# Kernel optimization log

Hardware: AMD Instinct MI355X
Metric: run time of the kernel (lower is better)

## Reference

```python
import jax, jax.numpy as jnp
import numpy as np

N = 50000      # nodes
E = 800000     # edges (avg degree 16)
F_IN = 128
HID = 128
C = 40
EPS = 1e-5     # BatchNorm1d eps


def setup_inputs() -> dict:
    key = jax.random.key(0)
    ks = jax.random.split(key, 8)

    def glorot(k, shape):
        lim = np.sqrt(6.0 / (shape[0] + shape[1])).astype(np.float32)
        return jax.random.uniform(k, shape, jnp.float32, -lim, lim)

    inp = {
        "features": jax.random.normal(ks[0], (N, F_IN), jnp.float32),
        "edge_index": jax.random.randint(ks[1], (2, E), 0, N, jnp.int32),
        "W1": glorot(ks[2], (F_IN, HID)), "b1": jnp.zeros((HID,), jnp.float32),
        "gamma1": jnp.ones((HID,), jnp.float32), "beta1": jnp.zeros((HID,), jnp.float32),
        "W2": glorot(ks[3], (HID, HID)), "b2": jnp.zeros((HID,), jnp.float32),
        "gamma2": jnp.ones((HID,), jnp.float32), "beta2": jnp.zeros((HID,), jnp.float32),
        "W3": glorot(ks[4], (HID, C)), "b3": jnp.zeros((C,), jnp.float32),
    }
    return inp


def _gcn_norm(edge_index):
    # Add self-loops and compute symmetric normalization D^-1/2 (A+I) D^-1/2
    loops = jnp.arange(N, dtype=edge_index.dtype)
    src = jnp.concatenate([edge_index[0], loops])
    dst = jnp.concatenate([edge_index[1], loops])
    deg = jax.ops.segment_sum(jnp.ones((E + N,), jnp.float32), dst, num_segments=N)
    dinv = jax.lax.rsqrt(jnp.maximum(deg, 1.0))
    return src, dst, dinv[src] * dinv[dst]  # per-edge norm coefficient


def _gcn_conv(x, W, b, src, dst, norm):
    h = x @ W                                   # [N, out]
    msg = h[src] * norm[:, None]                # gather + scale, [E+N, out]
    return jax.ops.segment_sum(msg, dst, num_segments=N) + b


def _bn(x, gamma, beta):
    # training-mode BatchNorm1d over the node axis (biased variance)
    mu = jnp.mean(x, axis=0)
    var = jnp.mean(jnp.square(x - mu), axis=0)
    return (x - mu) * jax.lax.rsqrt(var + EPS) * gamma + beta


def reference(features, edge_index, W1, b1, gamma1, beta1, W2, b2, gamma2, beta2, W3, b3):
    src, dst, norm = _gcn_norm(edge_index)
    h = jax.nn.relu(_bn(_gcn_conv(features, W1, b1, src, dst, norm), gamma1, beta1))
    h = jax.nn.relu(_bn(_gcn_conv(h, W2, b2, src, dst, norm), gamma2, beta2))
    h = _gcn_conv(h, W3, b3, src, dst, norm)
    return jax.nn.log_softmax(h, axis=-1)
```

## Files before the change

kernel.cpp:

```cpp
#include <hip/hip_runtime.h>
#include <math.h>

#define FEAT 128
#define NCLS 40
#define BN_EPS 1e-5f
#define CAP 64

typedef unsigned short u16;
typedef unsigned int u32;
typedef __attribute__((ext_vector_type(8))) short bf16x8;
typedef __attribute__((ext_vector_type(4))) float f32x4;

__device__ inline u32 f2b2(float a, float b) {
    u32 ua = __float_as_uint(a), ub = __float_as_uint(b);
    ua = (ua + 0x7fffu + ((ua >> 16) & 1u)) >> 16;
    ub = (ub + 0x7fffu + ((ub >> 16) & 1u)) >> 16;
    return ua | (ub << 16);
}
__device__ inline u16 f2b1(float a) {
    u32 ua = __float_as_uint(a);
    return (u16)((ua + 0x7fffu + ((ua >> 16) & 1u)) >> 16);
}
__device__ inline float b2f(u16 u) { return __uint_as_float((u32)u << 16); }
__device__ inline float4 b4fv(ushort4 u) {
    return make_float4(b2f(u.x), b2f(u.y), b2f(u.z), b2f(u.w));
}
__device__ inline float blo(u32 u) { return __uint_as_float(u << 16); }
__device__ inline float bhi(u32 u) { return __uint_as_float(u & 0xffff0000u); }

__device__ inline void b8acc(uint4 u, float w, float* a) {
    a[0] = fmaf(w, blo(u.x), a[0]); a[1] = fmaf(w, bhi(u.x), a[1]);
    a[2] = fmaf(w, blo(u.y), a[2]); a[3] = fmaf(w, bhi(u.y), a[3]);
    a[4] = fmaf(w, blo(u.z), a[4]); a[5] = fmaf(w, bhi(u.z), a[5]);
    a[6] = fmaf(w, blo(u.w), a[6]); a[7] = fmaf(w, bhi(u.w), a[7]);
}


__device__ inline void stage_wt(const float* __restrict__ W, u16* Wt) {
    const float4* W4 = (const float4*)W;
#pragma unroll
    for (int i = 0; i < 16; ++i) {
        int li = threadIdx.x + i * 256;
        int k = li >> 5;
        int n0 = (li & 31) * 4;
        int s = k >> 5, quad = (k >> 3) & 3, koff = k & 7;
        int nt = n0 >> 4, nl0 = n0 & 15;
        int base = ((s * 8 + nt) * 64 + quad * 16) * 8 + koff;
        float4 w = W4[li];
        Wt[base + (nl0 + 0) * 8] = f2b1(w.x);
        Wt[base + (nl0 + 1) * 8] = f2b1(w.y);
        Wt[base + (nl0 + 2) * 8] = f2b1(w.z);
        Wt[base + (nl0 + 3) * 8] = f2b1(w.w);
    }
}

__global__ __launch_bounds__(256) void k_pack(const float* __restrict__ W1,
                                              const float* __restrict__ W2,
                                              u16* __restrict__ Wg) {
    const float* W = (blockIdx.x == 0) ? W1 : W2;
    stage_wt(W, Wg + (size_t)blockIdx.x * 128 * 128);
}

__device__ inline void mfma_core(const u16* __restrict__ Wt, const bf16x8* bfrag,
                                 u16* __restrict__ Y, int node, int M, int nl, int quad) {
    int lane = quad * 16 + nl;
    f32x4 acc[8];
#pragma unroll
    for (int nt = 0; nt < 8; ++nt) acc[nt] = (f32x4){0.f, 0.f, 0.f, 0.f};
#pragma unroll
    for (int s = 0; s < 4; ++s) {
#pragma unroll
        for (int nt = 0; nt < 8; ++nt) {
            uint4 aw = ((const uint4*)Wt)[(s * 8 + nt) * 64 + lane];
            bf16x8 af = *(bf16x8*)&aw;
            acc[nt] = __builtin_amdgcn_mfma_f32_16x16x32_bf16(af, bfrag[s], acc[nt], 0, 0, 0);
        }
    }
    if (node < M) {
#pragma unroll
        for (int nt = 0; nt < 8; ++nt) {
            uint2 o;
            o.x = f2b2(acc[nt][0], acc[nt][1]);
            o.y = f2b2(acc[nt][2], acc[nt][3]);
            *(uint2*)&Y[(size_t)node * 128 + nt * 16 + quad * 4] = o;
        }
    }
}


__global__ __launch_bounds__(256, 8) void k_l1_fill(
    const float* __restrict__ X, const u16* __restrict__ Wg, u16* __restrict__ Y, int M,
    const int* __restrict__ src, const int* __restrict__ dst,
    int* __restrict__ cnt, u16* __restrict__ col, int E,
    int gemmBlocks, int nchunks)
{
    if ((int)blockIdx.x < gemmBlocks) {
        int wv = threadIdx.x >> 6;
        int lane = threadIdx.x & 63;
        int nl = lane & 15, quad = lane >> 4;
        int node = blockIdx.x * 64 + wv * 16 + nl;

        bf16x8 bfrag[4];
        if (node < M) {
            const float4* xr = (const float4*)(X + (size_t)node * 128);
#pragma unroll
            for (int s = 0; s < 4; ++s) {
                float4 xa = xr[s * 8 + quad * 2];
                float4 xb = xr[s * 8 + quad * 2 + 1];
                uint4 bu;
                bu.x = f2b2(xa.x, xa.y); bu.y = f2b2(xa.z, xa.w);
                bu.z = f2b2(xb.x, xb.y); bu.w = f2b2(xb.z, xb.w);
                bfrag[s] = *(bf16x8*)&bu;
            }
        } else {
            uint4 z = make_uint4(0, 0, 0, 0);
#pragma unroll
            for (int s = 0; s < 4; ++s) bfrag[s] = *(bf16x8*)&z;
        }
        mfma_core(Wg, bfrag, Y, node, M, nl, quad);
    } else {
        int fb = blockIdx.x - gemmBlocks;
        int part = fb & 7;
        int chunk = fb >> 3;
        int lo = (int)(((long long)M * part) >> 3);
        int hi = (int)(((long long)M * (part + 1)) >> 3);
        int per = ((E + nchunks - 1) / nchunks + 7) & ~7;
        int e0 = chunk * per;
        int e1 = e0 + per; if (e1 > E) e1 = E;

        for (int eb = e0 + (int)threadIdx.x * 8; eb < e1; eb += 2048) {
            if (eb + 8 <= e1) {
                int4 da = *(const int4*)(dst + eb);
                int4 db = *(const int4*)(dst + eb + 4);
                int4 sa = *(const int4*)(src + eb);
                int4 sb = *(const int4*)(src + eb + 4);
                int dd[8] = {da.x, da.y, da.z, da.w, db.x, db.y, db.z, db.w};
                int ss[8] = {sa.x, sa.y, sa.z, sa.w, sb.x, sb.y, sb.z, sb.w};
#pragma unroll
                for (int k = 0; k < 8; ++k) {
                    int d = dd[k];
                    if (d >= lo && d < hi) {
                        int c = atomicAdd(&cnt[d], 1);
                        if (c < CAP) col[(size_t)d * CAP + c] = (u16)ss[k];
                    }
                }
            } else {
                for (int e = eb; e < e1; ++e) {
                    int d = dst[e];
                    if (d >= lo && d < hi) {
                        int c = atomicAdd(&cnt[d], 1);
                        if (c < CAP) col[(size_t)d * CAP + c] = (u16)src[e];
                    }
                }
            }
        }
    }
}


__global__ __launch_bounds__(256) void k_mfma_l2(
    const u16* __restrict__ X, const u16* __restrict__ Wg,
    const float* __restrict__ sums, const float* __restrict__ gamma,
    const float* __restrict__ beta, u16* __restrict__ Y, int M)
{
    __shared__ __align__(16) float scs[128], shs[128];

    if (threadIdx.x < 128) {
        int f = threadIdx.x;
        float inv_n = 1.f / (float)M;
        float mu = sums[f] * inv_n;
        float var = sums[128 + f] * inv_n - mu * mu;
        float rs = rsqrtf(var + BN_EPS);
        float sc = gamma[f] * rs;
        scs[f] = sc;
        shs[f] = beta[f] - mu * sc;
    }
    __syncthreads();

    int wv = threadIdx.x >> 6;
    int lane = threadIdx.x & 63;
    int nl = lane & 15, quad = lane >> 4;
    int node = blockIdx.x * 64 + wv * 16 + nl;

    bf16x8 bfrag[4];
    if (node < M) {
        const uint4* xr = (const uint4*)(X + (size_t)node * 128);
#pragma unroll
        for (int s = 0; s < 4; ++s) {
            int k0 = s * 32 + quad * 8;
            uint4 xu = xr[s * 4 + quad];
            float4 sc0 = *(const float4*)&scs[k0];
            float4 sc1 = *(const float4*)&scs[k0 + 4];
            float4 sh0 = *(const float4*)&shs[k0];
            float4 sh1 = *(const float4*)&shs[k0 + 4];
            float v0 = fmaxf(fmaf(blo(xu.x), sc0.x, sh0.x), 0.f);
            float v1 = fmaxf(fmaf(bhi(xu.x), sc0.y, sh0.y), 0.f);
            float v2 = fmaxf(fmaf(blo(xu.y), sc0.z, sh0.z), 0.f);
            float v3 = fmaxf(fmaf(bhi(xu.y), sc0.w, sh0.w), 0.f);
            float v4 = fmaxf(fmaf(blo(xu.z), sc1.x, sh1.x), 0.f);
            float v5 = fmaxf(fmaf(bhi(xu.z), sc1.y, sh1.y), 0.f);
            float v6 = fmaxf(fmaf(blo(xu.w), sc1.z, sh1.z), 0.f);
            float v7 = fmaxf(fmaf(bhi(xu.w), sc1.w, sh1.w), 0.f);
            uint4 bu;
            bu.x = f2b2(v0, v1); bu.y = f2b2(v2, v3);
            bu.z = f2b2(v4, v5); bu.w = f2b2(v6, v7);
            bfrag[s] = *(bf16x8*)&bu;
        }
    } else {
        uint4 z = make_uint4(0, 0, 0, 0);
#pragma unroll
        for (int s = 0; s < 4; ++s) bfrag[s] = *(bf16x8*)&z;
    }
    mfma_core(Wg, bfrag, Y, node, M, nl, quad);
}


__global__ __launch_bounds__(256) void k_gemm40(
    const u16* __restrict__ X, const float* __restrict__ W,
    const float* __restrict__ sums, const float* __restrict__ gamma,
    const float* __restrict__ beta, u16* __restrict__ Y, int M)
{
    __shared__ float Ws[128 * 40];
    __shared__ __align__(16) float scs[128], shs[128];
    __shared__ float Xs[32 * 260];

    int t = threadIdx.x;
    int row0 = blockIdx.x * 256;
    int tx = t & 3, ty = t >> 2;

    if (t < 128) {
        float inv_n = 1.f / (float)M;
        float mu = sums[t] * inv_n;
        float var = sums[128 + t] * inv_n - mu * mu;
        float rs = rsqrtf(var + BN_EPS);
        float sc = gamma[t] * rs;
        scs[t] = sc;
        shs[t] = beta[t] - mu * sc;
    }
    {
        const float4* W4 = (const float4*)W;
        float4* Ws4 = (float4*)Ws;
#pragma unroll
        for (int i = 0; i < 5; ++i) Ws4[t + i * 256] = W4[t + i * 256];
    }

    float acc[4][10];
#pragma unroll
    for (int r = 0; r < 4; ++r)
#pragma unroll
        for (int c = 0; c < 10; ++c) acc[r][c] = 0.f;

    for (int k0 = 0; k0 < 128; k0 += 32) {
        __syncthreads();
        {
            int rr = t >> 3;
            int kc = (t & 7) * 4;
            float4 sc = *(const float4*)&scs[k0 + kc];
            float4 sh = *(const float4*)&shs[k0 + kc];
#pragma unroll
            for (int p = 0; p < 8; ++p) {
                int r = rr + p * 32;
                int grow = row0 + r;
                float4 v = make_float4(0.f, 0.f, 0.f, 0.f);
                if (grow < M) v = b4fv(*(const ushort4*)(X + (size_t)grow * 128 + k0 + kc));
                v.x = fmaxf(fmaf(v.x, sc.x, sh.x), 0.f);
                v.y = fmaxf(fmaf(v.y, sc.y, sh.y), 0.f);
                v.z = fmaxf(fmaf(v.z, sc.z, sh.z), 0.f);
                v.w = fmaxf(fmaf(v.w, sc.w, sh.w), 0.f);
                Xs[(kc + 0) * 260 + r] = v.x;
                Xs[(kc + 1) * 260 + r] = v.y;
                Xs[(kc + 2) * 260 + r] = v.z;
                Xs[(kc + 3) * 260 + r] = v.w;
            }
        }
        __syncthreads();
#pragma unroll 8
        for (int kk = 0; kk < 32; ++kk) {
            const float4 xv = *(const float4*)&Xs[kk * 260 + ty * 4];
            const float xr[4] = {xv.x, xv.y, xv.z, xv.w};
            float wc[10];
#pragma unroll
            for (int c = 0; c < 5; ++c) {
                float2 w2 = *(const float2*)&Ws[(k0 + kk) * 40 + tx * 10 + c * 2];
                wc[c * 2] = w2.x; wc[c * 2 + 1] = w2.y;
            }
#pragma unroll
            for (int r = 0; r < 4; ++r)
#pragma unroll
                for (int c = 0; c < 10; ++c)
                    acc[r][c] = fmaf(xr[r], wc[c], acc[r][c]);
        }
    }

#pragma unroll
    for (int r = 0; r < 4; ++r) {
        int grow = row0 + ty * 4 + r;
        if (grow < M) {
            u32* yp = (u32*)(Y + (size_t)grow * 40 + tx * 10);
#pragma unroll
            for (int c = 0; c < 5; ++c)
                yp[c] = f2b2(acc[r][c * 2], acc[r][c * 2 + 1]);
        }
    }
}


__global__ __launch_bounds__(256) void k_agg128(
    const u16* __restrict__ t, const int* __restrict__ cnt,
    const u16* __restrict__ col, const float* __restrict__ bias,
    u16* __restrict__ out, int n)
{
    int wid = threadIdx.x >> 4;
    int lane = threadIdx.x & 15;
    int i = blockIdx.x * 16 + wid;
    if (i >= n) return;
    int c = cnt[i];
    int deg = c < CAP ? c : CAP;
    int beg = i * CAP, end = beg + deg;
    float di = rsqrtf((float)(c + 1));

    float a[8];
    {
        uint4 su = ((const uint4*)(t + (size_t)i * 128))[lane];
        a[0] = di * blo(su.x); a[1] = di * bhi(su.x);
        a[2] = di * blo(su.y); a[3] = di * bhi(su.y);
        a[4] = di * blo(su.z); a[5] = di * bhi(su.z);
        a[6] = di * blo(su.w); a[7] = di * bhi(su.w);
    }

    int j = beg;
    for (; j + 7 < end; j += 8) {
        int s[8]; int sc[8]; uint4 v[8];
#pragma unroll
        for (int k = 0; k < 8; ++k) s[k] = (int)col[j + k];
#pragma unroll
        for (int k = 0; k < 8; ++k) {
            sc[k] = cnt[s[k]];
            v[k] = ((const uint4*)(t + (size_t)s[k] * 128))[lane];
        }
#pragma unroll
        for (int k = 0; k < 8; ++k) b8acc(v[k], rsqrtf((float)(sc[k] + 1)), a);
    }
    for (; j < end; ++j) {
        int s0 = (int)col[j];
        float w0 = rsqrtf((float)(cnt[s0] + 1));
        uint4 v = ((const uint4*)(t + (size_t)s0 * 128))[lane];
        b8acc(v, w0, a);
    }

    float4 bA = ((const float4*)bias)[lane * 2];
    float4 bB = ((const float4*)bias)[lane * 2 + 1];
    uint4 o;
    o.x = f2b2(fmaf(di, a[0], bA.x), fmaf(di, a[1], bA.y));
    o.y = f2b2(fmaf(di, a[2], bA.z), fmaf(di, a[3], bA.w));
    o.z = f2b2(fmaf(di, a[4], bB.x), fmaf(di, a[5], bB.y));
    o.w = f2b2(fmaf(di, a[6], bB.z), fmaf(di, a[7], bB.w));
    ((uint4*)(out + (size_t)i * 128))[lane] = o;
}


__global__ __launch_bounds__(256) void k_bnstats(const u16* __restrict__ a,
                                                 float* __restrict__ sums, int n) {
    int lane = threadIdx.x & 15;
    int rt = threadIdx.x >> 4;
    float s[8], q[8];
#pragma unroll
    for (int k = 0; k < 8; ++k) { s[k] = 0.f; q[k] = 0.f; }

    for (int i = blockIdx.x * 16 + rt; i < n; i += gridDim.x * 16) {
        uint4 u = ((const uint4*)(a + (size_t)i * 128))[lane];
        float v[8] = {blo(u.x), bhi(u.x), blo(u.y), bhi(u.y),
                      blo(u.z), bhi(u.z), blo(u.w), bhi(u.w)};
#pragma unroll
        for (int k = 0; k < 8; ++k) { s[k] += v[k]; q[k] = fmaf(v[k], v[k], q[k]); }
    }

    __shared__ float red[16][128];
#pragma unroll
    for (int k = 0; k < 8; ++k) red[rt][lane * 8 + k] = s[k];
    __syncthreads();
    if (threadIdx.x < 128) {
        float v = 0.f;
#pragma unroll
        for (int w = 0; w < 16; ++w) v += red[w][threadIdx.x];
        atomicAdd(&sums[threadIdx.x], v);
    }
    __syncthreads();
#pragma unroll
    for (int k = 0; k < 8; ++k) red[rt][lane * 8 + k] = q[k];
    __syncthreads();
    if (threadIdx.x < 128) {
        float v = 0.f;
#pragma unroll
        for (int w = 0; w < 16; ++w) v += red[w][threadIdx.x];
        atomicAdd(&sums[128 + threadIdx.x], v);
    }
}


__global__ __launch_bounds__(256) void k_agg40(
    const u16* __restrict__ t, const int* __restrict__ cnt,
    const u16* __restrict__ col, const float* __restrict__ bias,
    float* __restrict__ out, int n)
{
    int i = blockIdx.x * 32 + (threadIdx.x >> 3);
    if (i >= n) return;
    int l = threadIdx.x & 7;
    bool act = l < 5;
    int c = cnt[i];
    int deg = c < CAP ? c : CAP;
    int beg = i * CAP, end = beg + deg;
    float di = rsqrtf((float)(c + 1));

    float a[8] = {0.f, 0.f, 0.f, 0.f, 0.f, 0.f, 0.f, 0.f};
    if (act) {
        uint4 su = ((const uint4*)(t + (size_t)i * NCLS))[l];
        a[0] = di * blo(su.x); a[1] = di * bhi(su.x);
        a[2] = di * blo(su.y); a[3] = di * bhi(su.y);
        a[4] = di * blo(su.z); a[5] = di * bhi(su.z);
        a[6] = di * blo(su.w); a[7] = di * bhi(su.w);
    }
    int j = beg;
    for (; j + 7 < end; j += 8) {
        int s[8]; int sc[8]; uint4 v[8];
#pragma unroll
        for (int k = 0; k < 8; ++k) s[k] = (int)col[j + k];
#pragma unroll
        for (int k = 0; k < 8; ++k) {
            sc[k] = cnt[s[k]];
            v[k] = act ? ((const uint4*)(t + (size_t)s[k] * NCLS))[l]
                       : make_uint4(0, 0, 0, 0);
        }
#pragma unroll
        for (int k = 0; k < 8; ++k) b8acc(v[k], rsqrtf((float)(sc[k] + 1)), a);
    }
    for (; j < end; ++j) {
        int s0 = (int)col[j];
        float w0 = rsqrtf((float)(cnt[s0] + 1));
        uint4 v = act ? ((const uint4*)(t + (size_t)s0 * NCLS))[l]
                      : make_uint4(0, 0, 0, 0);
        b8acc(v, w0, a);
    }

    float v[8];
    float m = -INFINITY;
    if (act) {
        float4 b0 = *(const float4*)(bias + l * 8);
        float4 b1 = *(const float4*)(bias + l * 8 + 4);
        v[0] = fmaf(di, a[0], b0.x); v[1] = fmaf(di, a[1], b0.y);
        v[2] = fmaf(di, a[2], b0.z); v[3] = fmaf(di, a[3], b0.w);
        v[4] = fmaf(di, a[4], b1.x); v[5] = fmaf(di, a[5], b1.y);
        v[6] = fmaf(di, a[6], b1.z); v[7] = fmaf(di, a[7], b1.w);
#pragma unroll
        for (int k = 0; k < 8; ++k) m = fmaxf(m, v[k]);
    }
#pragma unroll
    for (int d = 1; d < 8; d <<= 1) m = fmaxf(m, __shfl_xor(m, d, 8));
    float es = 0.f;
    if (act) {
#pragma unroll
        for (int k = 0; k < 8; ++k) es += expf(v[k] - m);
    }
#pragma unroll
    for (int d = 1; d < 8; d <<= 1) es += __shfl_xor(es, d, 8);
    float ls = logf(es);
    if (act) {
        float4 o0, o1;
        o0.x = v[0] - m - ls; o0.y = v[1] - m - ls;
        o0.z = v[2] - m - ls; o0.w = v[3] - m - ls;
        o1.x = v[4] - m - ls; o1.y = v[5] - m - ls;
        o1.z = v[6] - m - ls; o1.w = v[7] - m - ls;
        *(float4*)(out + (size_t)i * NCLS + l * 8) = o0;
        *(float4*)(out + (size_t)i * NCLS + l * 8 + 4) = o1;
    }
}


extern "C" void kernel_launch(void* const* d_in, const int* in_sizes, int n_in,
                              void* d_out, int out_size, void* d_ws, size_t ws_size,
                              hipStream_t stream) {
    const float* features = (const float*)d_in[0];
    const int* edge_index = (const int*)d_in[1];
    const float* W1 = (const float*)d_in[2];
    const float* b1 = (const float*)d_in[3];
    const float* gamma1 = (const float*)d_in[4];
    const float* beta1 = (const float*)d_in[5];
    const float* W2 = (const float*)d_in[6];
    const float* b2 = (const float*)d_in[7];
    const float* gamma2 = (const float*)d_in[8];
    const float* beta2 = (const float*)d_in[9];
    const float* W3 = (const float*)d_in[10];
    const float* b3 = (const float*)d_in[11];
    float* out = (float*)d_out;

    int n = in_sizes[0] / FEAT;
    int E = in_sizes[1] / 2;

    char* p = (char*)d_ws;
    auto alloc = [&](size_t bytes) -> void* {
        void* r = (void*)p;
        p += (bytes + 255) & ~(size_t)255;
        return r;
    };
    int* cnt     = (int*)alloc((size_t)n * 4);
    float* sums  = (float*)alloc(512 * 4);
    size_t zspan = (size_t)((char*)(sums + 512) - (char*)cnt);
    u16* colb    = (u16*)alloc((size_t)n * CAP * 2);
    u16* hb      = (u16*)alloc((size_t)n * 128 * 2);
    u16* ab      = (u16*)alloc((size_t)n * 128 * 2);
    u16* wgb     = (u16*)alloc((size_t)2 * 128 * 128 * 2);

    float* sums1 = sums;
    float* sums2 = sums + 256;
    u16* Wg1 = wgb;
    u16* Wg2 = wgb + 128 * 128;

    const int* e_src = edge_index;
    const int* e_dst = edge_index + E;

    int gb64 = (n + 63) / 64;
    int gb16 = (n + 15) / 16;
    int gb32 = (n + 31) / 32;

    hipMemsetAsync(cnt, 0, zspan, stream);
    k_pack<<<2, 256, 0, stream>>>(W1, W2, wgb);

    int nchunks = 160;
    k_l1_fill<<<gb64 + nchunks * 8, 256, 0, stream>>>(features, Wg1, hb, n,
                                                      e_src, e_dst, cnt, colb, E,
                                                      gb64, nchunks);

    k_agg128<<<gb16, 256, 0, stream>>>(hb, cnt, colb, b1, ab, n);
    k_bnstats<<<512, 256, 0, stream>>>(ab, sums1, n);

    k_mfma_l2<<<gb64, 256, 0, stream>>>(ab, Wg2, sums1, gamma1, beta1, hb, n);
    k_agg128<<<gb16, 256, 0, stream>>>(hb, cnt, colb, b2, ab, n);
    k_bnstats<<<512, 256, 0, stream>>>(ab, sums2, n);

    k_gemm40<<<(n + 255) / 256, 256, 0, stream>>>(ab, W3, sums2, gamma2, beta2, hb, n);
    k_agg40<<<gb32, 256, 0, stream>>>(hb, cnt, colb, b3, out, n);
}
```

Baseline: 332.0 us.

## Fuse BN stats into aggregation, MFMA layer-3 GEMM, merge init kernels

BatchNorm sum and sum-of-squares accumulation moves into the 128-wide aggregation kernel, which becomes grid-stride over a capped grid. This drops the separate stats pass that re-read the activations. The fp32 scalar layer-3 GEMM is replaced by a bf16 MFMA kernel using a pre-packed, zero-padded W3. The memset and weight packing are merged into one init kernel, and layer-2 weights are staged in LDS. The capped grid reduces parallelism in the aggregation and adds more atomic contention per block, and bf16 on layer 3 changes numerics slightly.

```diff
diff --git a/kernel.cpp b/kernel.cpp
--- a/kernel.cpp
+++ b/kernel.cpp
@@ -22,9 +22,6 @@
     return (u16)((ua + 0x7fffu + ((ua >> 16) & 1u)) >> 16);
 }
 __device__ inline float b2f(u16 u) { return __uint_as_float((u32)u << 16); }
-__device__ inline float4 b4fv(ushort4 u) {
-    return make_float4(b2f(u.x), b2f(u.y), b2f(u.z), b2f(u.w));
-}
 __device__ inline float blo(u32 u) { return __uint_as_float(u << 16); }
 __device__ inline float bhi(u32 u) { return __uint_as_float(u & 0xffff0000u); }
 
@@ -54,14 +51,35 @@
     }
 }
 
-__global__ __launch_bounds__(256) void k_pack(const float* __restrict__ W1,
-                                              const float* __restrict__ W2,
-                                              u16* __restrict__ Wg) {
-    const float* W = (blockIdx.x == 0) ? W1 : W2;
-    stage_wt(W, Wg + (size_t)blockIdx.x * 128 * 128);
-}
-
-__device__ inline void mfma_core(const u16* __restrict__ Wt, const bf16x8* bfrag,
+__device__ inline void stage_wt40(const float* __restrict__ W, u16* Wt) {
+    for (int e = threadIdx.x; e < 12 * 64 * 8; e += 256) {
+        int j = e & 7;
+        int lane = (e >> 3) & 63;
+        int tile = e >> 9;
+        int s = tile / 3, nt = tile % 3;
+        int n = nt * 16 + (lane & 15);
+        int k = s * 32 + (lane >> 4) * 8 + j;
+        float v = (n < NCLS) ? W[k * NCLS + n] : 0.f;
+        Wt[e] = f2b1(v);
+    }
+}
+
+__global__ __launch_bounds__(256) void k_init(
+    const float* __restrict__ W1, const float* __restrict__ W2,
+    const float* __restrict__ W3, u16* __restrict__ Wg,
+    uint4* __restrict__ zbase, int zcount)
+{
+    int b = blockIdx.x;
+    if (b == 0) stage_wt(W1, Wg);
+    else if (b == 1) stage_wt(W2, Wg + 128 * 128);
+    else if (b == 2) stage_wt40(W3, Wg + 2 * 128 * 128);
+    else {
+        int idx = (b - 3) * 256 + threadIdx.x;
+        if (idx < zcount) zbase[idx] = make_uint4(0, 0, 0, 0);
+    }
+}
+
+__device__ inline void mfma_core(const uint4* __restrict__ wt4, const bf16x8* bfrag,
                                  u16* __restrict__ Y, int node, int M, int nl, int quad) {
     int lane = quad * 16 + nl;
     f32x4 acc[8];
@@ -71,7 +89,7 @@
     for (int s = 0; s < 4; ++s) {
 #pragma unroll
         for (int nt = 0; nt < 8; ++nt) {
-            uint4 aw = ((const uint4*)Wt)[(s * 8 + nt) * 64 + lane];
+            uint4 aw = wt4[(s * 8 + nt) * 64 + lane];
             bf16x8 af = *(bf16x8*)&aw;
             acc[nt] = __builtin_amdgcn_mfma_f32_16x16x32_bf16(af, bfrag[s], acc[nt], 0, 0, 0);
         }
@@ -117,7 +135,7 @@
 #pragma unroll
             for (int s = 0; s < 4; ++s) bfrag[s] = *(bf16x8*)&z;
         }
-        mfma_core(Wg, bfrag, Y, node, M, nl, quad);
+        mfma_core((const uint4*)Wg, bfrag, Y, node, M, nl, quad);
     } else {
         int fb = blockIdx.x - gemmBlocks;
         int part = fb & 7;
@@ -163,6 +181,7 @@
     const float* __restrict__ sums, const float* __restrict__ gamma,
     const float* __restrict__ beta, u16* __restrict__ Y, int M)
 {
+    __shared__ __align__(16) u16 Wt[128 * 128];
     __shared__ __align__(16) float scs[128], shs[128];
 
     if (threadIdx.x < 128) {
@@ -174,6 +193,12 @@
         float sc = gamma[f] * rs;
         scs[f] = sc;
         shs[f] = beta[f] - mu * sc;
+    }
+    {
+        uint4* d4 = (uint4*)Wt;
+        const uint4* s4 = (const uint4*)Wg;
+#pragma unroll
+        for (int i = 0; i < 8; ++i) d4[threadIdx.x + i * 256] = s4[threadIdx.x + i * 256];
     }
     __syncthreads();
 
@@ -211,173 +236,170 @@
 #pragma unroll
         for (int s = 0; s < 4; ++s) bfrag[s] = *(bf16x8*)&z;
     }
-    mfma_core(Wg, bfrag, Y, node, M, nl, quad);
-}
-
-
-__global__ __launch_bounds__(256) void k_gemm40(
-    const u16* __restrict__ X, const float* __restrict__ W,
+    mfma_core((const uint4*)Wt, bfrag, Y, node, M, nl, quad);
+}
+
+
+__global__ __launch_bounds__(256) void k_mfma_l3(
+    const u16* __restrict__ X, const u16* __restrict__ Wg,
     const float* __restrict__ sums, const float* __restrict__ gamma,
     const float* __restrict__ beta, u16* __restrict__ Y, int M)
 {
-    __shared__ float Ws[128 * 40];
+    __shared__ __align__(16) u16 Wt[12 * 64 * 8];
     __shared__ __align__(16) float scs[128], shs[128];
-    __shared__ float Xs[32 * 260];
-
-    int t = threadIdx.x;
-    int row0 = blockIdx.x * 256;
-    int tx = t & 3, ty = t >> 2;
-
-    if (t < 128) {
+
+    if (threadIdx.x < 128) {
+        int f = threadIdx.x;
         float inv_n = 1.f / (float)M;
-        float mu = sums[t] * inv_n;
-        float var = sums[128 + t] * inv_n - mu * mu;
+        float mu = sums[f] * inv_n;
+        float var = sums[128 + f] * inv_n - mu * mu;
         float rs = rsqrtf(var + BN_EPS);
-        float sc = gamma[t] * rs;
-        scs[t] = sc;
-        shs[t] = beta[t] - mu * sc;
+        float sc = gamma[f] * rs;
+        scs[f] = sc;
+        shs[f] = beta[f] - mu * sc;
     }
     {
-        const float4* W4 = (const float4*)W;
-        float4* Ws4 = (float4*)Ws;
-#pragma unroll
-        for (int i = 0; i < 5; ++i) Ws4[t + i * 256] = W4[t + i * 256];
-    }
-
-    float acc[4][10];
-#pragma unroll
-    for (int r = 0; r < 4; ++r)
-#pragma unroll
-        for (int c = 0; c < 10; ++c) acc[r][c] = 0.f;
-
-    for (int k0 = 0; k0 < 128; k0 += 32) {
-        __syncthreads();
-        {
-            int rr = t >> 3;
-            int kc = (t & 7) * 4;
-            float4 sc = *(const float4*)&scs[k0 + kc];
-            float4 sh = *(const float4*)&shs[k0 + kc];
-#pragma unroll
-            for (int p = 0; p < 8; ++p) {
-                int r = rr + p * 32;
-                int grow = row0 + r;
-                float4 v = make_float4(0.f, 0.f, 0.f, 0.f);
-                if (grow < M) v = b4fv(*(const ushort4*)(X + (size_t)grow * 128 + k0 + kc));
-                v.x = fmaxf(fmaf(v.x, sc.x, sh.x), 0.f);
-                v.y = fmaxf(fmaf(v.y, sc.y, sh.y), 0.f);
-                v.z = fmaxf(fmaf(v.z, sc.z, sh.z), 0.f);
-                v.w = fmaxf(fmaf(v.w, sc.w, sh.w), 0.f);
-                Xs[(kc + 0) * 260 + r] = v.x;
-                Xs[(kc + 1) * 260 + r] = v.y;
-                Xs[(kc + 2) * 260 + r] = v.z;
-                Xs[(kc + 3) * 260 + r] = v.w;
-            }
-        }
-        __syncthreads();
-#pragma unroll 8
-        for (int kk = 0; kk < 32; ++kk) {
-            const float4 xv = *(const float4*)&Xs[kk * 260 + ty * 4];
-            const float xr[4] = {xv.x, xv.y, xv.z, xv.w};
-            float wc[10];
-#pragma unroll
-            for (int c = 0; c < 5; ++c) {
-                float2 w2 = *(const float2*)&Ws[(k0 + kk) * 40 + tx * 10 + c * 2];
-                wc[c * 2] = w2.x; wc[c * 2 + 1] = w2.y;
-            }
-#pragma unroll
-            for (int r = 0; r < 4; ++r)
-#pragma unroll
-                for (int c = 0; c < 10; ++c)
-                    acc[r][c] = fmaf(xr[r], wc[c], acc[r][c]);
-        }
-    }
-
-#pragma unroll
-    for (int r = 0; r < 4; ++r) {
-        int grow = row0 + ty * 4 + r;
-        if (grow < M) {
-            u32* yp = (u32*)(Y + (size_t)grow * 40 + tx * 10);
-#pragma unroll
-            for (int c = 0; c < 5; ++c)
-                yp[c] = f2b2(acc[r][c * 2], acc[r][c * 2 + 1]);
-        }
-    }
-}
-
-
-__global__ __launch_bounds__(256) void k_agg128(
+        uint4* d4 = (uint4*)Wt;
+        const uint4* s4 = (const uint4*)Wg;
+#pragma unroll
+        for (int i = 0; i < 3; ++i) d4[threadIdx.x + i * 256] = s4[threadIdx.x + i * 256];
+    }
+    __syncthreads();
+
+    int wv = threadIdx.x >> 6;
+    int lane = threadIdx.x & 63;
+    int nl = lane & 15, quad = lane >> 4;
+    int node = blockIdx.x * 64 + wv * 16 + nl;
+
+    bf16x8 bfrag[4];
+    if (node < M) {
+        const uint4* xr = (const uint4*)(X + (size_t)node * 128);
+#pragma unroll
+        for (int s = 0; s < 4; ++s) {
+            int k0 = s * 32 + quad * 8;
+            uint4 xu = xr[s * 4 + quad];
+            float4 sc0 = *(const float4*)&scs[k0];
+            float4 sc1 = *(const float4*)&scs[k0 + 4];
+            float4 sh0 = *(const float4*)&shs[k0];
+            float4 sh1 = *(const float4*)&shs[k0 + 4];
+            float v0 = fmaxf(fmaf(blo(xu.x), sc0.x, sh0.x), 0.f);
+            float v1 = fmaxf(fmaf(bhi(xu.x), sc0.y, sh0.y), 0.f);
+            float v2 = fmaxf(fmaf(blo(xu.y), sc0.z, sh0.z), 0.f);
+            float v3 = fmaxf(fmaf(bhi(xu.y), sc0.w, sh0.w), 0.f);
+            float v4 = fmaxf(fmaf(blo(xu.z), sc1.x, sh1.x), 0.f);
+            float v5 = fmaxf(fmaf(bhi(xu.z), sc1.y, sh1.y), 0.f);
+            float v6 = fmaxf(fmaf(blo(xu.w), sc1.z, sh1.z), 0.f);
+            float v7 = fmaxf(fmaf(bhi(xu.w), sc1.w, sh1.w), 0.f);
+            uint4 bu;
+            bu.x = f2b2(v0, v1); bu.y = f2b2(v2, v3);
+            bu.z = f2b2(v4, v5); bu.w = f2b2(v6, v7);
+            bfrag[s] = *(bf16x8*)&bu;
+        }
+    } else {
+        uint4 z = make_uint4(0, 0, 0, 0);
+#pragma unroll
+        for (int s = 0; s < 4; ++s) bfrag[s] = *(bf16x8*)&z;
+    }
+
+    const uint4* wt4 = (const uint4*)Wt;
+    f32x4 acc[3];
+#pragma unroll
+    for (int nt = 0; nt < 3; ++nt) acc[nt] = (f32x4){0.f, 0.f, 0.f, 0.f};
+#pragma unroll
+    for (int s = 0; s < 4; ++s) {
+#pragma unroll
+        for (int nt = 0; nt < 3; ++nt) {
+            uint4 aw = wt4[(s * 3 + nt) * 64 + lane];
+            bf16x8 af = *(bf16x8*)&aw;
+            acc[nt] = __builtin_amdgcn_mfma_f32_16x16x32_bf16(af, bfrag[s], acc[nt], 0, 0, 0);
+        }
+    }
+    if (node < M) {
+#pragma unroll
+        for (int nt = 0; nt < 3; ++nt) {
+            int c0 = nt * 16 + quad * 4;
+            if (c0 < NCLS) {
+                uint2 o;
+                o.x = f2b2(acc[nt][0], acc[nt][1]);
+                o.y = f2b2(acc[nt][2], acc[nt][3]);
+                *(uint2*)&Y[(size_t)node * NCLS + c0] = o;
+            }
+        }
+    }
+}
+
+
+__global__ __launch_bounds__(256) void k_agg128_bn(
     const u16* __restrict__ t, const int* __restrict__ cnt,
     const u16* __restrict__ col, const float* __restrict__ bias,
-    u16* __restrict__ out, int n)
+    u16* __restrict__ out, float* __restrict__ sums, int n)
 {
     int wid = threadIdx.x >> 4;
     int lane = threadIdx.x & 15;
-    int i = blockIdx.x * 16 + wid;
-    if (i >= n) return;
-    int c = cnt[i];
-    int deg = c < CAP ? c : CAP;
-    int beg = i * CAP, end = beg + deg;
-    float di = rsqrtf((float)(c + 1));
-
-    float a[8];
-    {
-        uint4 su = ((const uint4*)(t + (size_t)i * 128))[lane];
-        a[0] = di * blo(su.x); a[1] = di * bhi(su.x);
-        a[2] = di * blo(su.y); a[3] = di * bhi(su.y);
-        a[4] = di * blo(su.z); a[5] = di * bhi(su.z);
-        a[6] = di * blo(su.w); a[7] = di * bhi(su.w);
-    }
-
-    int j = beg;
-    for (; j + 7 < end; j += 8) {
-        int s[8]; int sc[8]; uint4 v[8];
-#pragma unroll
-        for (int k = 0; k < 8; ++k) s[k] = (int)col[j + k];
-#pragma unroll
-        for (int k = 0; k < 8; ++k) {
-            sc[k] = cnt[s[k]];
-            v[k] = ((const uint4*)(t + (size_t)s[k] * 128))[lane];
-        }
-#pragma unroll
-        for (int k = 0; k < 8; ++k) b8acc(v[k], rsqrtf((float)(sc[k] + 1)), a);
-    }
-    for (; j < end; ++j) {
-        int s0 = (int)col[j];
-        float w0 = rsqrtf((float)(cnt[s0] + 1));
-        uint4 v = ((const uint4*)(t + (size_t)s0 * 128))[lane];
-        b8acc(v, w0, a);
-    }
-
     float4 bA = ((const float4*)bias)[lane * 2];
     float4 bB = ((const float4*)bias)[lane * 2 + 1];
-    uint4 o;
-    o.x = f2b2(fmaf(di, a[0], bA.x), fmaf(di, a[1], bA.y));
-    o.y = f2b2(fmaf(di, a[2], bA.z), fmaf(di, a[3], bA.w));
-    o.z = f2b2(fmaf(di, a[4], bB.x), fmaf(di, a[5], bB.y));
-    o.w = f2b2(fmaf(di, a[6], bB.z), fmaf(di, a[7], bB.w));
-    ((uint4*)(out + (size_t)i * 128))[lane] = o;
-}
-
-
-__global__ __launch_bounds__(256) void k_bnstats(const u16* __restrict__ a,
-                                                 float* __restrict__ sums, int n) {
-    int lane = threadIdx.x & 15;
-    int rt = threadIdx.x >> 4;
-    float s[8], q[8];
-#pragma unroll
-    for (int k = 0; k < 8; ++k) { s[k] = 0.f; q[k] = 0.f; }
-
-    for (int i = blockIdx.x * 16 + rt; i < n; i += gridDim.x * 16) {
-        uint4 u = ((const uint4*)(a + (size_t)i * 128))[lane];
-        float v[8] = {blo(u.x), bhi(u.x), blo(u.y), bhi(u.y),
-                      blo(u.z), bhi(u.z), blo(u.w), bhi(u.w)};
-#pragma unroll
-        for (int k = 0; k < 8; ++k) { s[k] += v[k]; q[k] = fmaf(v[k], v[k], q[k]); }
+
+    float bs[8], bq[8];
+#pragma unroll
+    for (int k = 0; k < 8; ++k) { bs[k] = 0.f; bq[k] = 0.f; }
+
+    for (int i0 = blockIdx.x * 16; i0 < n; i0 += gridDim.x * 16) {
+        int i = i0 + wid;
+        if (i < n) {
+            int c = cnt[i];
+            int deg = c < CAP ? c : CAP;
+            int beg = i * CAP, end = beg + deg;
+            float di = rsqrtf((float)(c + 1));
+
+            float a[8];
+            {
+                uint4 su = ((const uint4*)(t + (size_t)i * 128))[lane];
+                a[0] = di * blo(su.x); a[1] = di * bhi(su.x);
+                a[2] = di * blo(su.y); a[3] = di * bhi(su.y);
+                a[4] = di * blo(su.z); a[5] = di * bhi(su.z);
+                a[6] = di * blo(su.w); a[7] = di * bhi(su.w);
+            }
+
+            int j = beg;
+            for (; j + 7 < end; j += 8) {
+                int s[8]; int sc[8]; uint4 v[8];
+#pragma unroll
+                for (int k = 0; k < 8; ++k) s[k] = (int)col[j + k];
+#pragma unroll
+                for (int k = 0; k < 8; ++k) {
+                    sc[k] = cnt[s[k]];
+                    v[k] = ((const uint4*)(t + (size_t)s[k] * 128))[lane];
+                }
+#pragma unroll
+                for (int k = 0; k < 8; ++k) b8acc(v[k], rsqrtf((float)(sc[k] + 1)), a);
+            }
+            for (; j < end; ++j) {
+                int s0 = (int)col[j];
+                float w0 = rsqrtf((float)(cnt[s0] + 1));
+                uint4 v = ((const uint4*)(t + (size_t)s0 * 128))[lane];
+                b8acc(v, w0, a);
+            }
+
+            float vv[8];
+            vv[0] = fmaf(di, a[0], bA.x); vv[1] = fmaf(di, a[1], bA.y);
+            vv[2] = fmaf(di, a[2], bA.z); vv[3] = fmaf(di, a[3], bA.w);
+            vv[4] = fmaf(di, a[4], bB.x); vv[5] = fmaf(di, a[5], bB.y);
+            vv[6] = fmaf(di, a[6], bB.z); vv[7] = fmaf(di, a[7], bB.w);
+            uint4 o;
+            o.x = f2b2(vv[0], vv[1]); o.y = f2b2(vv[2], vv[3]);
+            o.z = f2b2(vv[4], vv[5]); o.w = f2b2(vv[6], vv[7]);
+            ((uint4*)(out + (size_t)i * 128))[lane] = o;
+#pragma unroll
+            for (int k = 0; k < 8; ++k) {
+                bs[k] += vv[k];
+                bq[k] = fmaf(vv[k], vv[k], bq[k]);
+            }
+        }
     }
 
     __shared__ float red[16][128];
 #pragma unroll
-    for (int k = 0; k < 8; ++k) red[rt][lane * 8 + k] = s[k];
+    for (int k = 0; k < 8; ++k) red[wid][lane * 8 + k] = bs[k];
     __syncthreads();
     if (threadIdx.x < 128) {
         float v = 0.f;
@@ -387,7 +409,7 @@
     }
     __syncthreads();
 #pragma unroll
-    for (int k = 0; k < 8; ++k) red[rt][lane * 8 + k] = q[k];
+    for (int k = 0; k < 8; ++k) red[wid][lane * 8 + k] = bq[k];
     __syncthreads();
     if (threadIdx.x < 128) {
         float v = 0.f;
@@ -508,12 +530,13 @@
     u16* colb    = (u16*)alloc((size_t)n * CAP * 2);
     u16* hb      = (u16*)alloc((size_t)n * 128 * 2);
     u16* ab      = (u16*)alloc((size_t)n * 128 * 2);
-    u16* wgb     = (u16*)alloc((size_t)2 * 128 * 128 * 2);
+    u16* wgb     = (u16*)alloc((size_t)(2 * 128 * 128 + 12 * 64 * 8) * 2);
 
     float* sums1 = sums;
     float* sums2 = sums + 256;
     u16* Wg1 = wgb;
     u16* Wg2 = wgb + 128 * 128;
+    u16* Wg3 = wgb + 2 * 128 * 128;
 
     const int* e_src = edge_index;
     const int* e_dst = edge_index + E;
@@ -521,22 +544,22 @@
     int gb64 = (n + 63) / 64;
     int gb16 = (n + 15) / 16;
     int gb32 = (n + 31) / 32;
-
-    hipMemsetAsync(cnt, 0, zspan, stream);
-    k_pack<<<2, 256, 0, stream>>>(W1, W2, wgb);
+    int aggGrid = gb16 < 1024 ? gb16 : 1024;
+
+    int zcount = (int)(zspan / 16);
+    int zblocks = (zcount + 255) / 256;
+    k_init<<<3 + zblocks, 256, 0, stream>>>(W1, W2, W3, wgb, (uint4*)cnt, zcount);
 
     int nchunks = 160;
     k_l1_fill<<<gb64 + nchunks * 8, 256, 0, stream>>>(features, Wg1, hb, n,
                                                       e_src, e_dst, cnt, colb, E,
                                                       gb64, nchunks);
 
-    k_agg128<<<gb16, 256, 0, stream>>>(hb, cnt, colb, b1, ab, n);
-    k_bnstats<<<512, 256, 0, stream>>>(ab, sums1, n);
+    k_agg128_bn<<<aggGrid, 256, 0, stream>>>(hb, cnt, colb, b1, ab, sums1, n);
 
     k_mfma_l2<<<gb64, 256, 0, stream>>>(ab, Wg2, sums1, gamma1, beta1, hb, n);
-    k_agg128<<<gb16, 256, 0, stream>>>(hb, cnt, colb, b2, ab, n);
-    k_bnstats<<<512, 256, 0, stream>>>(ab, sums2, n);
-
-    k_gemm40<<<(n + 255) / 256, 256, 0, stream>>>(ab, W3, sums2, gamma2, beta2, hb, n);
+    k_agg128_bn<<<aggGrid, 256, 0, stream>>>(hb, cnt, colb, b2, ab, sums2, n);
+
+    k_mfma_l3<<<gb64, 256, 0, stream>>>(ab, Wg3, sums2, gamma2, beta2, hb, n);
     k_agg40<<<gb32, 256, 0, stream>>>(hb, cnt, colb, b3, out, n);
 }
```

After: 299.7 us. 1.11x faster.
